# Performance work log

Measured on AMD Instinct MI355X. Metric: run time of the kernel, lower is better.

Reference implementation:

```python
import jax, jax.numpy as jnp
import numpy as np

B, T, I, H = 512, 64, 128, 128
E = I - 1  # encoder_in


def _cell(x, h, c, Wih, Whh, bih, bhh):
    # PyTorch LSTM gate order: i, f, g, o
    g = x @ Wih.T + h @ Whh.T + bih + bhh
    i, f, gg, o = jnp.split(g, 4, axis=-1)
    c2 = jax.nn.sigmoid(f) * c + jax.nn.sigmoid(i) * jnp.tanh(gg)
    h2 = jax.nn.sigmoid(o) * jnp.tanh(c2)
    return h2, c2


def setup_inputs() -> dict:
    key = jax.random.key(0)
    ks = iter(jax.random.split(key, 40))
    n = lambda *s: jax.random.normal(next(ks), s, dtype=jnp.float32) * 0.05
    inp = {
        'input_data': jax.random.normal(next(ks), (B, T, I), dtype=jnp.float32),
        # encoder LSTM (2 layers, input E)
        'enc_Wih0': n(4 * H, E), 'enc_Whh0': n(4 * H, H), 'enc_bih0': n(4 * H), 'enc_bhh0': n(4 * H),
        'enc_Wih1': n(4 * H, H), 'enc_Whh1': n(4 * H, H), 'enc_bih1': n(4 * H), 'enc_bhh1': n(4 * H),
        # decoder LSTM (2 layers, input 1)
        'dec_Wih0': n(4 * H, 1), 'dec_Whh0': n(4 * H, H), 'dec_bih0': n(4 * H), 'dec_bhh0': n(4 * H),
        'dec_Wih1': n(4 * H, H), 'dec_Whh1': n(4 * H, H), 'dec_bih1': n(4 * H), 'dec_bhh1': n(4 * H),
        # input attention MLP: (2H+T)->T->1
        'attn_W1': n(T, 2 * H + T), 'attn_b1': n(T), 'attn_W2': n(1, T), 'attn_b2': n(1),
        # temporal attention MLP: 3H->H->1
        'attnd_W1': n(H, 3 * H), 'attnd_b1': n(H), 'attnd_W2': n(1, H), 'attnd_b2': n(1),
        # decoder input projection (H+1)->1 and output projection 2H->1
        'decin_W': n(1, H + 1), 'decin_b': n(1),
        'proj_W': n(1, 2 * H), 'proj_b': n(1),
    }
    return inp


def reference(input_data, enc_Wih0, enc_Whh0, enc_bih0, enc_bhh0,
              enc_Wih1, enc_Whh1, enc_bih1, enc_bhh1,
              dec_Wih0, dec_Whh0, dec_bih0, dec_bhh0,
              dec_Wih1, dec_Whh1, dec_bih1, dec_bhh1,
              attn_W1, attn_b1, attn_W2, attn_b2,
              attnd_W1, attnd_b1, attnd_W2, attnd_b2,
              decin_W, decin_b, proj_W, proj_b):
    b, t, i = input_data.shape
    e, hdim = i - 1, enc_Whh0.shape[1]
    inp_enc = input_data[:, :, 1:]              # [B,T,E]
    inp_dec = input_data[:, :, 0]               # [B,T]
    inp_perm = jnp.transpose(inp_enc, (0, 2, 1))  # [B,E,T]
    z = jnp.zeros((b, hdim), input_data.dtype)

    def enc_step(carry, x_t):
        h0, c0, h1, c1 = carry
        hc = jnp.concatenate([
            jnp.broadcast_to(h1[:, None, :], (b, e, hdim)),
            jnp.broadcast_to(c1[:, None, :], (b, e, hdim)),
            inp_perm], axis=-1)                              # [B,E,2H+T]
        logits = jnp.tanh(hc @ attn_W1.T + attn_b1) @ attn_W2.T + attn_b2
        a = jax.nn.softmax(logits[..., 0], axis=-1)          # [B,E]
        h0, c0 = _cell(x_t * a, h0, c0, enc_Wih0, enc_Whh0, enc_bih0, enc_bhh0)
        h1, c1 = _cell(h0, h1, c1, enc_Wih1, enc_Whh1, enc_bih1, enc_bhh1)
        return (h0, c0, h1, c1), h1

    _, h_top = jax.lax.scan(enc_step, (z, z, z, z), jnp.transpose(inp_enc, (1, 0, 2)))
    h_exp = jnp.transpose(h_top, (1, 0, 2))  # [B,T,H]

    def dec_step(carry, x_t):
        h0, c0, h1, c1, _ = carry
        hc = jnp.concatenate([
            jnp.broadcast_to(h1[:, None, :], (b, t, hdim)),
            jnp.broadcast_to(c1[:, None, :], (b, t, hdim)),
            h_exp], axis=-1)                                  # [B,T,3H]
        logits = jnp.tanh(hc @ attnd_W1.T + attnd_b1) @ attnd_W2.T + attnd_b2
        a = jax.nn.softmax(logits[..., 0], axis=-1)           # [B,T]
        partial = jnp.einsum('bth,bt->bh', h_exp, a)          # [B,H]
        full = jnp.concatenate([partial, x_t[:, None]], axis=-1)  # [B,H+1]
        din = full @ decin_W.T + decin_b                      # [B,1]
        h0, c0 = _cell(din, h0, c0, dec_Wih0, dec_Whh0, dec_bih0, dec_bhh0)
        h1, c1 = _cell(h0, h1, c1, dec_Wih1, dec_Whh1, dec_bih1, dec_bhh1)
        return (h0, c0, h1, c1, partial), None

    (h0, c0, h1, c1, partial), _ = jax.lax.scan(dec_step, (z, z, z, z, z), jnp.transpose(inp_dec))
    out = jnp.concatenate([h1, partial], axis=-1) @ proj_W.T + proj_b  # [B,1]
    return out
```

## Files before the change

kernel.cpp:

```cpp
#include <hip/hip_runtime.h>

#define BATCH 512
#define TT 64
#define II 128

#define OFF_Wr_e0 0
#define OFF_Wr_e1 (OFF_Wr_e0 + 512*256)
#define OFF_Wr_d1 (OFF_Wr_e1 + 512*256)
#define OFF_bs0e  (OFF_Wr_d1 + 512*256)
#define OFF_bs1e  (OFF_bs0e + 512)
#define OFF_bs0d  (OFF_bs1e + 512)
#define OFF_bs1d  (OFF_bs0d + 512)
#define OFF_xprojT (OFF_bs1d + 512)
#define OFF_hexp   (OFF_xprojT + BATCH*8192)
#define OFF_hprojT (OFF_hexp + BATCH*8192)

struct Params {
  const float* input;
  const float *eWih0, *eWhh0, *ebih0, *ebhh0, *eWih1, *eWhh1, *ebih1, *ebhh1;
  const float *dWih0, *dWhh0, *dbih0, *dbhh0, *dWih1, *dWhh1, *dbih1, *dbhh1;
  const float *aW1, *ab1, *aW2, *ab2;
  const float *adW1, *adb1, *adW2, *adb2;
  const float *dinW, *dinb, *projW, *projb;
  float* ws;
  float* out;
};

#define L2E 1.4426950408889634f

__device__ __forceinline__ float exp2f_(float x){ return __builtin_amdgcn_exp2f(x); }
__device__ __forceinline__ float rcp_(float x){ return __builtin_amdgcn_rcpf(x); }
__device__ __forceinline__ float fast_tanh(float x){
  float t = exp2f_(x * 2.8853900817779268f);
  return 1.f - 2.f * rcp_(t + 1.f);
}
__device__ __forceinline__ float sigm(float x){
  return rcp_(1.f + exp2f_(-x * L2E));
}
__device__ __forceinline__ float wave_max(float v){
  #pragma unroll
  for (int o = 32; o > 0; o >>= 1) v = fmaxf(v, __shfl_xor(v, o, 64));
  return v;
}
__device__ __forceinline__ float wave_sum(float v){
  #pragma unroll
  for (int o = 32; o > 0; o >>= 1) v += __shfl_xor(v, o, 64);
  return v;
}

#define DOT(A,W,X) A += (W).x*(X).x + (W).y*(X).y + (W).z*(X).z + (W).w*(X).w;

__global__ __launch_bounds__(256) void k_prep(Params p){
  float* ws = p.ws;
  const int gid = blockIdx.x*256 + threadIdx.x;
  const int gsz = gridDim.x*256;
  for (int i = gid; i < 512*256; i += gsz){
    const int j = i >> 8, k = i & 255;
    ws[OFF_Wr_e0 + i] = (k < 128) ? ((k < 127) ? p.eWih0[j*127 + k] : 0.f)
                                  : p.eWhh0[j*128 + (k-128)];
    ws[OFF_Wr_e1 + i] = (k < 128) ? p.eWih1[j*128 + k] : p.eWhh1[j*128 + (k-128)];
    ws[OFF_Wr_d1 + i] = (k < 128) ? p.dWih1[j*128 + k] : p.dWhh1[j*128 + (k-128)];
  }
  for (int i = gid; i < 512; i += gsz){
    ws[OFF_bs0e+i] = p.ebih0[i]+p.ebhh0[i];
    ws[OFF_bs1e+i] = p.ebih1[i]+p.ebhh1[i];
    ws[OFF_bs0d+i] = p.dbih0[i]+p.dbhh0[i];
    ws[OFF_bs1d+i] = p.dbih1[i]+p.dbhh1[i];
  }
}

__global__ __launch_bounds__(256) void k_xproj(Params p){
  __shared__ float xin[64][128];
  __shared__ float w1x[64][64];
  __shared__ float b1s[64];
  const int b = blockIdx.x, tid = threadIdx.x;
  const float* inb = p.input + (size_t)b*(TT*II);
  for (int i = tid; i < 64*128; i += 256){
    const int k = i >> 7, e = i & 127;
    xin[k][e] = (e < 127) ? inb[k*II + 1 + e] : 0.f;
  }
  for (int i = tid; i < 64*64; i += 256){
    const int j = i >> 6, k = i & 63;
    w1x[j][k] = p.aW1[j*320 + 256 + k];
  }
  if (tid < 64) b1s[tid] = p.ab1[tid];
  __syncthreads();
  float* outb = p.ws + OFF_xprojT + (size_t)b*8192;
  for (int i = tid; i < 64*128; i += 256){
    const int j = i >> 7, e = i & 127;
    float acc = b1s[j];
    #pragma unroll 8
    for (int k = 0; k < 64; ++k) acc += xin[k][e] * w1x[j][k];
    outb[i] = acc;
  }
}

__global__ __launch_bounds__(256) void k_hproj(Params p){
  __shared__ float hx[64][129];
  __shared__ float bs[128];
  const int b = blockIdx.x, tid = threadIdx.x;
  const float* hb = p.ws + OFF_hexp + (size_t)b*8192;
  for (int i = tid; i < 64*128; i += 256) hx[i>>7][i&127] = hb[i];
  if (tid < 128) bs[tid] = p.adb1[tid];
  __syncthreads();
  float* outb = p.ws + OFF_hprojT + (size_t)b*8192;
  for (int i = tid; i < 128*64; i += 256){
    const int kk = i >> 6, t2 = i & 63;
    const float* w = p.adW1 + kk*384 + 256;
    float acc = bs[kk];
    #pragma unroll 8
    for (int k = 0; k < 128; ++k) acc += hx[t2][k] * w[k];
    outb[i] = acc;
  }
}

#define ENC_LDS_FLOATS (16384+1024+256+1024+1024+128+64+8+8)
__global__ __launch_bounds__(512) void k_enc(Params p){
  extern __shared__ float sm[];
  float* xp   = sm;
  float* Se   = xp + 16384;
  float* c0s  = Se + 1024;
  float* gpA  = c0s + 256;
  float* gpB  = gpA + 1024;
  float* g01s = gpB + 1024;
  float* w2   = g01s + 128;
  float* pm   = w2 + 64;
  float* psu  = pm + 8;
  const int tid = threadIdx.x;
  const int b0 = blockIdx.x*2;
  float* ws = p.ws;

  { const float4* xsrc = (const float4*)(ws + OFF_xprojT + (size_t)b0*8192);
    float4* xdst = (float4*)xp;
    for (int i = tid; i < 4096; i += 512) xdst[i] = xsrc[i]; }
  for (int i = tid; i < 1024; i += 512) Se[i] = 0.f;
  if (tid < 256) c0s[tid] = 0.f;
  if (tid < 64) w2[tid] = p.aW2[tid];
  const float b2 = p.ab2[0];

  const int kqE = tid & 3, oE = tid >> 2, jjE = oE & 63, bbE = oE >> 6;
  const int jh2 = tid & 1, o2 = tid >> 1, e2 = o2 & 127, bb2 = o2 >> 7;
  const int qtr = (tid >> 6) & 3;
  const int jg = tid & 255, khg = tid >> 8;
  const int uu = tid & 127, bbu = (tid >> 7) & 1;

  const float bias0a = ws[OFF_bs0e + jg], bias0b = ws[OFF_bs0e + 256 + jg];
  const float bias1a = ws[OFF_bs1e + jg], bias1b = ws[OFF_bs1e + 256 + jg];
  const float* wE1 = p.aW1 + jjE*320 + kqE*64;
  const float* wE3 = ws + OFF_Wr_e0 + jg*256 + khg*128;
  const float* wE4 = ws + OFF_Wr_e1 + jg*256 + khg*128;
  __syncthreads();

  for (int t = 0; t < TT; ++t){
    {
      const float* xbase = Se + bbE*512 + 256 + kqE*64;
      float a = 0.f;
      #pragma unroll
      for (int kg = 0; kg < 16; ++kg){
        const int idx = (((kg + kqE*4 + bbE*2) & 15) << 2);
        const float4 w = *(const float4*)(wE1 + idx);
        const float4 x = *(const float4*)(xbase + idx);
        DOT(a,w,x)
      }
      a += __shfl_xor(a,1,64); a += __shfl_xor(a,2,64);
      if (kqE == 0) g01s[bbE*64 + jjE] = a;
    }
    __syncthreads();
    float accL;
    {
      const float* xpe = xp + bb2*8192 + e2;
      const float* gg = g01s + bb2*64 + jh2*32;
      const float* w2p = w2 + jh2*32;
      float a = 0.f;
      #pragma unroll 8
      for (int q = 0; q < 32; ++q)
        a += w2p[q] * fast_tanh(xpe[(jh2*32+q)*128] + gg[q]);
      a += __shfl_xor(a,1,64);
      a += b2;
      if (e2 == 127) a = -3.0e38f;
      accL = a;
      const float m = wave_max(a);
      const float pe = exp2f_((a - m)*L2E);
      const float s = wave_sum(pe)*0.5f;
      if ((tid & 63) == 0){ pm[bb2*4+qtr] = m; psu[bb2*4+qtr] = s; }
    }
    __syncthreads();
    {
      const float m0=pm[bb2*4],m1=pm[bb2*4+1],m2=pm[bb2*4+2],m3=pm[bb2*4+3];
      const float gm = fmaxf(fmaxf(m0,m1),fmaxf(m2,m3));
      const float tot = psu[bb2*4]*exp2f_((m0-gm)*L2E) + psu[bb2*4+1]*exp2f_((m1-gm)*L2E)
                      + psu[bb2*4+2]*exp2f_((m2-gm)*L2E) + psu[bb2*4+3]*exp2f_((m3-gm)*L2E);
      const float aa = exp2f_((accL-gm)*L2E)*rcp_(tot);
      float xv = 0.f;
      if (e2 < 127) xv = p.input[(size_t)(b0+bb2)*8192 + t*128 + 1 + e2] * aa;
      Se[bb2*512 + e2] = xv;
    }
    __syncthreads();
    {
      const float* ob0 = Se + khg*128;
      const float* ob1 = Se + 512 + khg*128;
      float a00,a01,a10,a11;
      a00 = a01 = khg ? 0.f : bias0a;
      a10 = a11 = khg ? 0.f : bias0b;
      #pragma unroll 8
      for (int kg = 0; kg < 32; ++kg){
        const float4 w  = *(const float4*)(wE3 + kg*4);
        const float4 w2_= *(const float4*)(wE3 + 65536 + kg*4);
        const float4 x0 = *(const float4*)(ob0 + kg*4);
        const float4 x1 = *(const float4*)(ob1 + kg*4);
        DOT(a00,w,x0) DOT(a01,w,x1) DOT(a10,w2_,x0) DOT(a11,w2_,x1)
      }
      float* gp = khg ? gpB : gpA;
      gp[jg] = a00; gp[512 + jg] = a01;
      gp[256 + jg] = a10; gp[768 + jg] = a11;
    }
    __syncthreads();
    if (tid < 256){
      const int base = bbu*512 + uu;
      const float gi = gpA[base] + gpB[base];
      const float gf = gpA[base+128] + gpB[base+128];
      const float gg2= gpA[base+256] + gpB[base+256];
      const float go = gpA[base+384] + gpB[base+384];
      const float c = sigm(gf)*c0s[tid] + sigm(gi)*fast_tanh(gg2);
      c0s[tid] = c;
      Se[bbu*512 + 128 + uu] = sigm(go)*fast_tanh(c);
    }
    __syncthreads();
    {
      const float* ob0 = Se + 128 + khg*128;
      const float* ob1 = Se + 640 + khg*128;
      float a00,a01,a10,a11;
      a00 = a01 = khg ? 0.f : bias1a;
      a10 = a11 = khg ? 0.f : bias1b;
      #pragma unroll 8
      for (int kg = 0; kg < 32; ++kg){
        const float4 w  = *(const float4*)(wE4 + kg*4);
        const float4 w2_= *(const float4*)(wE4 + 65536 + kg*4);
        const float4 x0 = *(const float4*)(ob0 + kg*4);
        const float4 x1 = *(const float4*)(ob1 + kg*4);
        DOT(a00,w,x0) DOT(a01,w,x1) DOT(a10,w2_,x0) DOT(a11,w2_,x1)
      }
      float* gp = khg ? gpB : gpA;
      gp[jg] = a00; gp[512 + jg] = a01;
      gp[256 + jg] = a10; gp[768 + jg] = a11;
    }
    __syncthreads();
    if (tid < 256){
      const int base = bbu*512 + uu;
      const float gi = gpA[base] + gpB[base];
      const float gf = gpA[base+128] + gpB[base+128];
      const float gg2= gpA[base+256] + gpB[base+256];
      const float go = gpA[base+384] + gpB[base+384];
      const float c = sigm(gf)*Se[bbu*512+384+uu] + sigm(gi)*fast_tanh(gg2);
      Se[bbu*512+384+uu] = c;
      const float h = sigm(go)*fast_tanh(c);
      Se[bbu*512+256+uu] = h;
      ws[OFF_hexp + (size_t)(b0+bbu)*8192 + t*128 + uu] = h;
    }
    __syncthreads();
  }
}

#define DEC_LDS_FLOATS (16640+768+256+1024+1024+256+128+8+8+8+128+256)
__global__ __launch_bounds__(512) void k_dec(Params p){
  extern __shared__ float sm[];
  float* hp    = sm;
  float* Sd    = hp + 16640;
  float* c0s   = Sd + 768;
  float* gpA   = c0s + 256;
  float* gpB   = gpA + 1024;
  float* g01d  = gpB + 1024;
  float* lraw  = g01d + 256;
  float* pm    = lraw + 128;
  float* psu   = pm + 8;
  float* dpart = psu + 8;
  float* wd2   = dpart + 8;
  float* parts = wd2 + 128;
  const int tid = threadIdx.x;
  const int b0 = blockIdx.x*2;
  float* ws = p.ws;

  { const float* hsrc = ws + OFF_hprojT + (size_t)b0*8192;
    for (int i = tid; i < 16384; i += 512){
      const int bb = i>>13, kk = (i>>6)&127, tl = i&63;
      hp[bb*8320 + kk*65 + tl] = hsrc[i];
    } }
  for (int i = tid; i < 768; i += 512) Sd[i] = 0.f;
  if (tid < 256) c0s[tid] = 0.f;
  if (tid < 128) wd2[tid] = p.adW2[tid];
  const float bd2 = p.adb2[0];

  const int kh1 = tid & 1, o1 = tid >> 1, kk1 = o1 & 127, bb1 = o1 >> 7;
  const int kqa = tid & 3, oa = tid >> 2, tla = oa & 63, bba = oa >> 6;
  const int qtr = (tid >> 6) & 3;
  const int thc = tid & 1, oc = tid >> 1, hc = oc & 127, bbc = oc >> 7;
  const int jg = tid & 255, khg = tid >> 8;
  const int uu = tid & 127, bbu = (tid >> 7) & 1;

  const float bias0da = ws[OFF_bs0d + jg], bias0db = ws[OFF_bs0d + 256 + jg];
  const float bias1da = ws[OFF_bs1d + jg], bias1db = ws[OFF_bs1d + 256 + jg];
  const float dW0a = p.dWih0[jg], dW0b = p.dWih0[256 + jg];
  const float dinw_hc = p.dinW[hc];
  const float dinw128 = p.dinW[128], dinbv = p.dinb[0];
  const float* wD1 = p.adW1 + kk1*384 + kh1*128;
  const float* wD3 = p.dWhh0 + jg*128 + khg*64;
  const float* wD4 = ws + OFF_Wr_d1 + jg*256 + khg*128;
  const float* heB = ws + OFF_hexp + (size_t)(b0+bbc)*8192 + hc;
  __syncthreads();

  for (int t = 0; t < TT; ++t){
    {
      const float* xbase = Sd + bb1*384 + 128 + kh1*128;
      float a = 0.f;
      #pragma unroll 8
      for (int kg = 0; kg < 32; ++kg){
        const int idx = (((kg + kh1*4 + bb1*2) & 31) << 2);
        const float4 w = *(const float4*)(wD1 + idx);
        const float4 x = *(const float4*)(xbase + idx);
        DOT(a,w,x)
      }
      a += __shfl_xor(a,1,64);
      if (kh1 == 0) g01d[bb1*128 + kk1] = a;
    }
    __syncthreads();
    {
      const float* hpb = hp + bba*8320 + tla;
      const float* gg = g01d + bba*128;
      float a = 0.f;
      #pragma unroll 8
      for (int q = 0; q < 32; ++q){
        const int kk = kqa*32 + ((q + kqa*8) & 31);
        a += wd2[kk] * fast_tanh(hpb[kk*65] + gg[kk]);
      }
      a += __shfl_xor(a,1,64); a += __shfl_xor(a,2,64);
      a += bd2;
      if (kqa == 0) lraw[bba*64 + tla] = a;
      const float m = wave_max(a);
      const float pe = exp2f_((a-m)*L2E);
      const float s = wave_sum(pe)*0.25f;
      if ((tid & 63) == 0){ pm[bba*4+qtr] = m; psu[bba*4+qtr] = s; }
    }
    __syncthreads();
    if (tid < 128){
      const int bb = tid >> 6;
      const float m0=pm[bb*4],m1=pm[bb*4+1],m2=pm[bb*4+2],m3=pm[bb*4+3];
      const float gm = fmaxf(fmaxf(m0,m1),fmaxf(m2,m3));
      const float tot = psu[bb*4]*exp2f_((m0-gm)*L2E)+psu[bb*4+1]*exp2f_((m1-gm)*L2E)
                      +psu[bb*4+2]*exp2f_((m2-gm)*L2E)+psu[bb*4+3]*exp2f_((m3-gm)*L2E);
      lraw[tid] = exp2f_((lraw[tid]-gm)*L2E)*rcp_(tot);
    }
    __syncthreads();
    {
      const float* av = lraw + bbc*64 + thc*32;
      float a = 0.f;
      #pragma unroll 8
      for (int q = 0; q < 32; ++q) a += av[q] * heB[(thc*32+q)*128];
      a += __shfl_xor(a,1,64);
      if (thc == 0) parts[bbc*128 + hc] = a;
      float v = a * dinw_hc;
      v = wave_sum(v)*0.5f;
      if ((tid & 63) == 0) dpart[bbc*4+qtr] = v;
    }
    __syncthreads();
    {
      const float dn0 = dpart[0]+dpart[1]+dpart[2]+dpart[3]
                      + p.input[(size_t)(b0+0)*8192 + t*128]*dinw128 + dinbv;
      const float dn1 = dpart[4]+dpart[5]+dpart[6]+dpart[7]
                      + p.input[(size_t)(b0+1)*8192 + t*128]*dinw128 + dinbv;
      const float* ob0 = Sd + khg*64;
      const float* ob1 = Sd + 384 + khg*64;
      float a00,a01,a10,a11;
      if (khg){ a00=a01=a10=a11=0.f; }
      else {
        a00 = bias0da + dn0*dW0a; a01 = bias0da + dn1*dW0a;
        a10 = bias0db + dn0*dW0b; a11 = bias0db + dn1*dW0b;
      }
      #pragma unroll 8
      for (int kg = 0; kg < 16; ++kg){
        const float4 w  = *(const float4*)(wD3 + kg*4);
        const float4 w2_= *(const float4*)(wD3 + 32768 + kg*4);
        const float4 x0 = *(const float4*)(ob0 + kg*4);
        const float4 x1 = *(const float4*)(ob1 + kg*4);
        DOT(a00,w,x0) DOT(a01,w,x1) DOT(a10,w2_,x0) DOT(a11,w2_,x1)
      }
      float* gp = khg ? gpB : gpA;
      gp[jg] = a00; gp[512 + jg] = a01;
      gp[256 + jg] = a10; gp[768 + jg] = a11;
    }
    __syncthreads();
    if (tid < 256){
      const int base = bbu*512 + uu;
      const float gi = gpA[base] + gpB[base];
      const float gf = gpA[base+128] + gpB[base+128];
      const float gg2= gpA[base+256] + gpB[base+256];
      const float go = gpA[base+384] + gpB[base+384];
      const float c = sigm(gf)*c0s[tid] + sigm(gi)*fast_tanh(gg2);
      c0s[tid] = c;
      Sd[bbu*384 + uu] = sigm(go)*fast_tanh(c);
    }
    __syncthreads();
    {
      const float* ob0 = Sd + khg*128;
      const float* ob1 = Sd + 384 + khg*128;
      float a00,a01,a10,a11;
      a00 = a01 = khg ? 0.f : bias1da;
      a10 = a11 = khg ? 0.f : bias1db;
      #pragma unroll 8
      for (int kg = 0; kg < 32; ++kg){
        const float4 w  = *(const float4*)(wD4 + kg*4);
        const float4 w2_= *(const float4*)(wD4 + 65536 + kg*4);
        const float4 x0 = *(const float4*)(ob0 + kg*4);
        const float4 x1 = *(const float4*)(ob1 + kg*4);
        DOT(a00,w,x0) DOT(a01,w,x1) DOT(a10,w2_,x0) DOT(a11,w2_,x1)
      }
      float* gp = khg ? gpB : gpA;
      gp[jg] = a00; gp[512 + jg] = a01;
      gp[256 + jg] = a10; gp[768 + jg] = a11;
    }
    __syncthreads();
    if (tid < 256){
      const int base = bbu*512 + uu;
      const float gi = gpA[base] + gpB[base];
      const float gf = gpA[base+128] + gpB[base+128];
      const float gg2= gpA[base+256] + gpB[base+256];
      const float go = gpA[base+384] + gpB[base+384];
      const float c = sigm(gf)*Sd[bbu*384+256+uu] + sigm(gi)*fast_tanh(gg2);
      Sd[bbu*384+256+uu] = c;
      Sd[bbu*384+128+uu] = sigm(go)*fast_tanh(c);
    }
    __syncthreads();
  }
  if (tid < 128){
    const int bb = tid>>6, l = tid&63;
    float v = Sd[bb*384+128+l]*p.projW[l] + Sd[bb*384+192+l]*p.projW[64+l]
            + parts[bb*128+l]*p.projW[128+l] + parts[bb*128+64+l]*p.projW[192+l];
    v = wave_sum(v);
    if (l == 0) p.out[b0 + bb] = v + p.projb[0];
  }
}

extern "C" void kernel_launch(void* const* d_in, const int* in_sizes, int n_in,
                              void* d_out, int out_size, void* d_ws, size_t ws_size,
                              hipStream_t stream){
  Params p;
  p.input = (const float*)d_in[0];
  p.eWih0=(const float*)d_in[1];  p.eWhh0=(const float*)d_in[2];
  p.ebih0=(const float*)d_in[3];  p.ebhh0=(const float*)d_in[4];
  p.eWih1=(const float*)d_in[5];  p.eWhh1=(const float*)d_in[6];
  p.ebih1=(const float*)d_in[7];  p.ebhh1=(const float*)d_in[8];
  p.dWih0=(const float*)d_in[9];  p.dWhh0=(const float*)d_in[10];
  p.dbih0=(const float*)d_in[11]; p.dbhh0=(const float*)d_in[12];
  p.dWih1=(const float*)d_in[13]; p.dWhh1=(const float*)d_in[14];
  p.dbih1=(const float*)d_in[15]; p.dbhh1=(const float*)d_in[16];
  p.aW1=(const float*)d_in[17];   p.ab1=(const float*)d_in[18];
  p.aW2=(const float*)d_in[19];   p.ab2=(const float*)d_in[20];
  p.adW1=(const float*)d_in[21];  p.adb1=(const float*)d_in[22];
  p.adW2=(const float*)d_in[23];  p.adb2=(const float*)d_in[24];
  p.dinW=(const float*)d_in[25];  p.dinb=(const float*)d_in[26];
  p.projW=(const float*)d_in[27]; p.projb=(const float*)d_in[28];
  p.ws = (float*)d_ws;
  p.out = (float*)d_out;

  (void)hipFuncSetAttribute(reinterpret_cast<const void*>(k_enc),
      hipFuncAttributeMaxDynamicSharedMemorySize, ENC_LDS_FLOATS*4);
  (void)hipFuncSetAttribute(reinterpret_cast<const void*>(k_dec),
      hipFuncAttributeMaxDynamicSharedMemorySize, DEC_LDS_FLOATS*4);

  hipLaunchKernelGGL(k_prep,  dim3(128), dim3(256), 0, stream, p);
  hipLaunchKernelGGL(k_xproj, dim3(BATCH), dim3(256), 0, stream, p);
  hipLaunchKernelGGL(k_enc,   dim3(256), dim3(512), ENC_LDS_FLOATS*4, stream, p);
  hipLaunchKernelGGL(k_hproj, dim3(BATCH), dim3(256), 0, stream, p);
  hipLaunchKernelGGL(k_dec,   dim3(256), dim3(512), DEC_LDS_FLOATS*4, stream, p);
}
```

Before: 4.872 ms.

## Hold recurrent LSTM weights in registers with one batch per 1024-thread block

The encoder and decoder recurrent kernels now handle one batch element per block with 1024 threads instead of two per 512-thread block. Each thread preloads its slice of the LSTM and attention weights into registers once, so the inner loops no longer re-read weights from global memory at every timestep. The decoder also stages h_exp in LDS instead of reading it from global memory. The cost is very high register pressure (about 68 float4 per thread), which risks spills and leaves little occupancy. Reductions are spread over more threads, with extra scratch passes through LDS.

```diff
diff --git a/kernel.cpp b/kernel.cpp
--- a/kernel.cpp
+++ b/kernel.cpp
@@ -114,328 +114,276 @@
   }
 }
 
-#define ENC_LDS_FLOATS (16384+1024+256+1024+1024+128+64+8+8)
-__global__ __launch_bounds__(512) void k_enc(Params p){
+#define ENC_LDS_FLOATS (8192+512+128+512+512+1024+64+64+2+2)
+__global__ __launch_bounds__(1024) void k_enc(Params p){
   extern __shared__ float sm[];
   float* xp   = sm;
-  float* Se   = xp + 16384;
-  float* c0s  = Se + 1024;
-  float* gpA  = c0s + 256;
-  float* gpB  = gpA + 1024;
-  float* g01s = gpB + 1024;
-  float* w2   = g01s + 128;
-  float* pm   = w2 + 64;
-  float* psu  = pm + 8;
+  float* Se   = xp + 8192;
+  float* c0s  = Se + 512;
+  float* gpA  = c0s + 128;
+  float* gpB  = gpA + 512;
+  float* scr  = gpB + 512;
+  float* g01  = scr + 1024;
+  float* w2s  = g01 + 64;
+  float* pm   = w2s + 64;
+  float* psu  = pm + 2;
   const int tid = threadIdx.x;
-  const int b0 = blockIdx.x*2;
+  const int b = blockIdx.x;
   float* ws = p.ws;
 
-  { const float4* xsrc = (const float4*)(ws + OFF_xprojT + (size_t)b0*8192);
-    float4* xdst = (float4*)xp;
-    for (int i = tid; i < 4096; i += 512) xdst[i] = xsrc[i]; }
-  for (int i = tid; i < 1024; i += 512) Se[i] = 0.f;
-  if (tid < 256) c0s[tid] = 0.f;
-  if (tid < 64) w2[tid] = p.aW2[tid];
+  { const float4* s = (const float4*)(ws + OFF_xprojT + (size_t)b*8192);
+    float4* d = (float4*)xp;
+    d[tid] = s[tid];
+    d[tid + 1024] = s[tid + 1024]; }
+  if (tid < 512) Se[tid] = 0.f;
+  if (tid < 128) c0s[tid] = 0.f;
+  if (tid < 64) w2s[tid] = p.aW2[tid];
   const float b2 = p.ab2[0];
 
-  const int kqE = tid & 3, oE = tid >> 2, jjE = oE & 63, bbE = oE >> 6;
-  const int jh2 = tid & 1, o2 = tid >> 1, e2 = o2 & 127, bb2 = o2 >> 7;
-  const int qtr = (tid >> 6) & 3;
-  const int jg = tid & 255, khg = tid >> 8;
-  const int uu = tid & 127, bbu = (tid >> 7) & 1;
-
-  const float bias0a = ws[OFF_bs0e + jg], bias0b = ws[OFF_bs0e + 256 + jg];
-  const float bias1a = ws[OFF_bs1e + jg], bias1b = ws[OFF_bs1e + 256 + jg];
-  const float* wE1 = p.aW1 + jjE*320 + kqE*64;
-  const float* wE3 = ws + OFF_Wr_e0 + jg*256 + khg*128;
-  const float* wE4 = ws + OFF_Wr_e1 + jg*256 + khg*128;
+  const int kqE = tid & 15, jjE = tid >> 4;
+  const int eA = tid & 127, jq = tid >> 7;
+  const int r = tid & 511, kh = tid >> 9;
+
+  float4 W1[4], W3[32], W4[32];
+  #pragma unroll
+  for (int i = 0; i < 4; ++i)
+    W1[i] = *(const float4*)(p.aW1 + jjE*320 + kqE*16 + ((i + kqE) & 3)*4);
+  #pragma unroll
+  for (int i = 0; i < 32; ++i)
+    W3[i] = *(const float4*)(ws + OFF_Wr_e0 + r*256 + kh*128 + i*4);
+  #pragma unroll
+  for (int i = 0; i < 32; ++i)
+    W4[i] = *(const float4*)(ws + OFF_Wr_e1 + r*256 + kh*128 + i*4);
+  const float bias0 = ws[OFF_bs0e + r];
+  const float bias1 = ws[OFF_bs1e + r];
+  const float* xrow = p.input + (size_t)b*8192;
   __syncthreads();
 
   for (int t = 0; t < TT; ++t){
-    {
-      const float* xbase = Se + bbE*512 + 256 + kqE*64;
-      float a = 0.f;
-      #pragma unroll
-      for (int kg = 0; kg < 16; ++kg){
-        const int idx = (((kg + kqE*4 + bbE*2) & 15) << 2);
-        const float4 w = *(const float4*)(wE1 + idx);
-        const float4 x = *(const float4*)(xbase + idx);
-        DOT(a,w,x)
+    float xreg = 0.f;
+    if (tid < 127) xreg = xrow[t*128 + 1 + tid];
+    {
+      const float4* X = (const float4*)(Se + 256) + kqE*4;
+      float a = 0.f;
+      #pragma unroll
+      for (int i = 0; i < 4; ++i){ const float4 x = X[(i + kqE) & 3]; DOT(a, W1[i], x) }
+      a += __shfl_xor(a,1,64); a += __shfl_xor(a,2,64);
+      a += __shfl_xor(a,4,64); a += __shfl_xor(a,8,64);
+      if (kqE == 0) g01[jjE] = a;
+    }
+    __syncthreads();
+    {
+      float a = 0.f;
+      #pragma unroll
+      for (int q = 0; q < 8; ++q){
+        const int j = jq*8 + q;
+        a += w2s[j] * fast_tanh(xp[j*128 + eA] + g01[j]);
       }
-      a += __shfl_xor(a,1,64); a += __shfl_xor(a,2,64);
-      if (kqE == 0) g01s[bbE*64 + jjE] = a;
-    }
-    __syncthreads();
-    float accL;
-    {
-      const float* xpe = xp + bb2*8192 + e2;
-      const float* gg = g01s + bb2*64 + jh2*32;
-      const float* w2p = w2 + jh2*32;
-      float a = 0.f;
-      #pragma unroll 8
-      for (int q = 0; q < 32; ++q)
-        a += w2p[q] * fast_tanh(xpe[(jh2*32+q)*128] + gg[q]);
-      a += __shfl_xor(a,1,64);
-      a += b2;
-      if (e2 == 127) a = -3.0e38f;
-      accL = a;
+      scr[jq*128 + eA] = a;
+    }
+    __syncthreads();
+    float aL = 0.f;
+    if (tid < 128){
+      aL = b2;
+      #pragma unroll
+      for (int q = 0; q < 8; ++q) aL += scr[q*128 + tid];
+      if (tid == 127) aL = -3.0e38f;
+      const float m = wave_max(aL);
+      const float pe = exp2f_((aL - m)*L2E);
+      const float s = wave_sum(pe);
+      if ((tid & 63) == 0){ pm[tid>>6] = m; psu[tid>>6] = s; }
+    }
+    __syncthreads();
+    if (tid < 128){
+      const float m0 = pm[0], m1 = pm[1];
+      const float gm = fmaxf(m0, m1);
+      const float tot = psu[0]*exp2f_((m0-gm)*L2E) + psu[1]*exp2f_((m1-gm)*L2E);
+      const float aa = exp2f_((aL-gm)*L2E)*rcp_(tot);
+      Se[tid] = (tid < 127) ? xreg*aa : 0.f;
+    }
+    __syncthreads();
+    {
+      float a = kh ? 0.f : bias0;
+      const float4* X = (const float4*)Se + kh*32;
+      #pragma unroll
+      for (int kg = 0; kg < 32; ++kg){ const float4 x = X[kg]; DOT(a, W3[kg], x) }
+      (kh ? gpB : gpA)[r] = a;
+    }
+    __syncthreads();
+    if (tid < 128){
+      const float gi = gpA[tid]+gpB[tid], gf = gpA[128+tid]+gpB[128+tid];
+      const float gg = gpA[256+tid]+gpB[256+tid], go = gpA[384+tid]+gpB[384+tid];
+      const float c = sigm(gf)*c0s[tid] + sigm(gi)*fast_tanh(gg);
+      c0s[tid] = c;
+      Se[128+tid] = sigm(go)*fast_tanh(c);
+    }
+    __syncthreads();
+    {
+      float a = kh ? 0.f : bias1;
+      const float4* X = (const float4*)Se + 32 + kh*32;
+      #pragma unroll
+      for (int kg = 0; kg < 32; ++kg){ const float4 x = X[kg]; DOT(a, W4[kg], x) }
+      (kh ? gpB : gpA)[r] = a;
+    }
+    __syncthreads();
+    if (tid < 128){
+      const float gi = gpA[tid]+gpB[tid], gf = gpA[128+tid]+gpB[128+tid];
+      const float gg = gpA[256+tid]+gpB[256+tid], go = gpA[384+tid]+gpB[384+tid];
+      const float c = sigm(gf)*Se[384+tid] + sigm(gi)*fast_tanh(gg);
+      Se[384+tid] = c;
+      const float h = sigm(go)*fast_tanh(c);
+      Se[256+tid] = h;
+      ws[OFF_hexp + (size_t)b*8192 + t*128 + tid] = h;
+    }
+    __syncthreads();
+  }
+}
+
+#define DEC_LDS_FLOATS (8320+8192+384+128+512+512+1024+128+64+128+2+128)
+__global__ __launch_bounds__(1024) void k_dec(Params p){
+  extern __shared__ float sm[];
+  float* hp    = sm;
+  float* hex   = hp + 8320;
+  float* Sd    = hex + 8192;
+  float* c0s   = Sd + 384;
+  float* gpA   = c0s + 128;
+  float* gpB   = gpA + 512;
+  float* scr   = gpB + 512;
+  float* g01d  = scr + 1024;
+  float* abuf  = g01d + 128;
+  float* parts = abuf + 64;
+  float* dpart = parts + 128;
+  float* wd2   = dpart + 2;
+  const int tid = threadIdx.x;
+  const int b = blockIdx.x;
+  float* ws = p.ws;
+
+  { const float* s = ws + OFF_hprojT + (size_t)b*8192;
+    #pragma unroll
+    for (int rep = 0; rep < 8; ++rep){
+      const int i = rep*1024 + tid;
+      hp[(i>>6)*65 + (i&63)] = s[i];
+    }
+    const float4* s2 = (const float4*)(ws + OFF_hexp + (size_t)b*8192);
+    ((float4*)hex)[tid] = s2[tid];
+    ((float4*)hex)[tid + 1024] = s2[tid + 1024];
+  }
+  if (tid < 384) Sd[tid] = 0.f;
+  if (tid < 128) c0s[tid] = 0.f;
+  if (tid < 128) wd2[tid] = p.adW2[tid];
+  const float bd2 = p.adb2[0];
+
+  const int kq8 = tid & 7, kkD = tid >> 3;
+  const int tA = tid & 63, kq16 = tid >> 6;
+  const int hC = tid & 127, tq = tid >> 7;
+  const int r = tid & 511, kh = tid >> 9;
+
+  float4 WD1[8], WD3[16], WD4[32];
+  #pragma unroll
+  for (int i = 0; i < 8; ++i)
+    WD1[i] = *(const float4*)(p.adW1 + kkD*384 + kq8*32 + ((i + kq8) & 7)*4);
+  #pragma unroll
+  for (int i = 0; i < 16; ++i)
+    WD3[i] = *(const float4*)(p.dWhh0 + r*128 + kh*64 + i*4);
+  #pragma unroll
+  for (int i = 0; i < 32; ++i)
+    WD4[i] = *(const float4*)(ws + OFF_Wr_d1 + r*256 + kh*128 + i*4);
+  const float bias0d = ws[OFF_bs0d + r];
+  const float bias1d = ws[OFF_bs1d + r];
+  const float dW0r = p.dWih0[r];
+  const float dinw_h = p.dinW[hC];
+  const float dinw128 = p.dinW[128], dinbv = p.dinb[0];
+  __syncthreads();
+
+  for (int t = 0; t < TT; ++t){
+    const float xd = p.input[(size_t)b*8192 + t*128];
+    {
+      const float4* X = (const float4*)(Sd + 128) + kq8*8;
+      float a = 0.f;
+      #pragma unroll
+      for (int i = 0; i < 8; ++i){ const float4 x = X[(i + kq8) & 7]; DOT(a, WD1[i], x) }
+      a += __shfl_xor(a,1,64); a += __shfl_xor(a,2,64); a += __shfl_xor(a,4,64);
+      if (kq8 == 0) g01d[kkD] = a;
+    }
+    __syncthreads();
+    {
+      float a = 0.f;
+      #pragma unroll
+      for (int q = 0; q < 8; ++q){
+        const int kk = kq16*8 + q;
+        a += wd2[kk] * fast_tanh(hp[kk*65 + tA] + g01d[kk]);
+      }
+      scr[kq16*64 + tA] = a;
+    }
+    __syncthreads();
+    if (tid < 64){
+      float a = bd2;
+      #pragma unroll
+      for (int q = 0; q < 16; ++q) a += scr[q*64 + tid];
       const float m = wave_max(a);
       const float pe = exp2f_((a - m)*L2E);
-      const float s = wave_sum(pe)*0.5f;
-      if ((tid & 63) == 0){ pm[bb2*4+qtr] = m; psu[bb2*4+qtr] = s; }
-    }
-    __syncthreads();
-    {
-      const float m0=pm[bb2*4],m1=pm[bb2*4+1],m2=pm[bb2*4+2],m3=pm[bb2*4+3];
-      const float gm = fmaxf(fmaxf(m0,m1),fmaxf(m2,m3));
-      const float tot = psu[bb2*4]*exp2f_((m0-gm)*L2E) + psu[bb2*4+1]*exp2f_((m1-gm)*L2E)
-                      + psu[bb2*4+2]*exp2f_((m2-gm)*L2E) + psu[bb2*4+3]*exp2f_((m3-gm)*L2E);
-      const float aa = exp2f_((accL-gm)*L2E)*rcp_(tot);
-      float xv = 0.f;
-      if (e2 < 127) xv = p.input[(size_t)(b0+bb2)*8192 + t*128 + 1 + e2] * aa;
-      Se[bb2*512 + e2] = xv;
-    }
-    __syncthreads();
-    {
-      const float* ob0 = Se + khg*128;
-      const float* ob1 = Se + 512 + khg*128;
-      float a00,a01,a10,a11;
-      a00 = a01 = khg ? 0.f : bias0a;
-      a10 = a11 = khg ? 0.f : bias0b;
-      #pragma unroll 8
-      for (int kg = 0; kg < 32; ++kg){
-        const float4 w  = *(const float4*)(wE3 + kg*4);
-        const float4 w2_= *(const float4*)(wE3 + 65536 + kg*4);
-        const float4 x0 = *(const float4*)(ob0 + kg*4);
-        const float4 x1 = *(const float4*)(ob1 + kg*4);
-        DOT(a00,w,x0) DOT(a01,w,x1) DOT(a10,w2_,x0) DOT(a11,w2_,x1)
+      abuf[tid] = pe * rcp_(wave_sum(pe));
+    }
+    __syncthreads();
+    {
+      float a = 0.f;
+      #pragma unroll
+      for (int q = 0; q < 8; ++q){
+        const int t2 = tq*8 + q;
+        a += abuf[t2] * hex[t2*128 + hC];
       }
-      float* gp = khg ? gpB : gpA;
-      gp[jg] = a00; gp[512 + jg] = a01;
-      gp[256 + jg] = a10; gp[768 + jg] = a11;
-    }
-    __syncthreads();
-    if (tid < 256){
-      const int base = bbu*512 + uu;
-      const float gi = gpA[base] + gpB[base];
-      const float gf = gpA[base+128] + gpB[base+128];
-      const float gg2= gpA[base+256] + gpB[base+256];
-      const float go = gpA[base+384] + gpB[base+384];
-      const float c = sigm(gf)*c0s[tid] + sigm(gi)*fast_tanh(gg2);
+      scr[tq*128 + hC] = a;
+    }
+    __syncthreads();
+    if (tid < 128){
+      float a = 0.f;
+      #pragma unroll
+      for (int q = 0; q < 8; ++q) a += scr[q*128 + tid];
+      parts[tid] = a;
+      float v = a * dinw_h;
+      v = wave_sum(v);
+      if ((tid & 63) == 0) dpart[tid>>6] = v;
+    }
+    __syncthreads();
+    {
+      const float dn = dpart[0] + dpart[1] + xd*dinw128 + dinbv;
+      float a = kh ? 0.f : (bias0d + dn*dW0r);
+      const float4* X = (const float4*)Sd + kh*16;
+      #pragma unroll
+      for (int kg = 0; kg < 16; ++kg){ const float4 x = X[kg]; DOT(a, WD3[kg], x) }
+      (kh ? gpB : gpA)[r] = a;
+    }
+    __syncthreads();
+    if (tid < 128){
+      const float gi = gpA[tid]+gpB[tid], gf = gpA[128+tid]+gpB[128+tid];
+      const float gg = gpA[256+tid]+gpB[256+tid], go = gpA[384+tid]+gpB[384+tid];
+      const float c = sigm(gf)*c0s[tid] + sigm(gi)*fast_tanh(gg);
       c0s[tid] = c;
-      Se[bbu*512 + 128 + uu] = sigm(go)*fast_tanh(c);
-    }
-    __syncthreads();
-    {
-      const float* ob0 = Se + 128 + khg*128;
-      const float* ob1 = Se + 640 + khg*128;
-      float a00,a01,a10,a11;
-      a00 = a01 = khg ? 0.f : bias1a;
-      a10 = a11 = khg ? 0.f : bias1b;
-      #pragma unroll 8
-      for (int kg = 0; kg < 32; ++kg){
-        const float4 w  = *(const float4*)(wE4 + kg*4);
-        const float4 w2_= *(const float4*)(wE4 + 65536 + kg*4);
-        const float4 x0 = *(const float4*)(ob0 + kg*4);
-        const float4 x1 = *(const float4*)(ob1 + kg*4);
-        DOT(a00,w,x0) DOT(a01,w,x1) DOT(a10,w2_,x0) DOT(a11,w2_,x1)
-      }
-      float* gp = khg ? gpB : gpA;
-      gp[jg] = a00; gp[512 + jg] = a01;
-      gp[256 + jg] = a10; gp[768 + jg] = a11;
-    }
-    __syncthreads();
-    if (tid < 256){
-      const int base = bbu*512 + uu;
-      const float gi = gpA[base] + gpB[base];
-      const float gf = gpA[base+128] + gpB[base+128];
-      const float gg2= gpA[base+256] + gpB[base+256];
-      const float go = gpA[base+384] + gpB[base+384];
-      const float c = sigm(gf)*Se[bbu*512+384+uu] + sigm(gi)*fast_tanh(gg2);
-      Se[bbu*512+384+uu] = c;
-      const float h = sigm(go)*fast_tanh(c);
-      Se[bbu*512+256+uu] = h;
-      ws[OFF_hexp + (size_t)(b0+bbu)*8192 + t*128 + uu] = h;
-    }
-    __syncthreads();
-  }
-}
-
-#define DEC_LDS_FLOATS (16640+768+256+1024+1024+256+128+8+8+8+128+256)
-__global__ __launch_bounds__(512) void k_dec(Params p){
-  extern __shared__ float sm[];
-  float* hp    = sm;
-  float* Sd    = hp + 16640;
-  float* c0s   = Sd + 768;
-  float* gpA   = c0s + 256;
-  float* gpB   = gpA + 1024;
-  float* g01d  = gpB + 1024;
-  float* lraw  = g01d + 256;
-  float* pm    = lraw + 128;
-  float* psu   = pm + 8;
-  float* dpart = psu + 8;
-  float* wd2   = dpart + 8;
-  float* parts = wd2 + 128;
-  const int tid = threadIdx.x;
-  const int b0 = blockIdx.x*2;
-  float* ws = p.ws;
-
-  { const float* hsrc = ws + OFF_hprojT + (size_t)b0*8192;
-    for (int i = tid; i < 16384; i += 512){
-      const int bb = i>>13, kk = (i>>6)&127, tl = i&63;
-      hp[bb*8320 + kk*65 + tl] = hsrc[i];
-    } }
-  for (int i = tid; i < 768; i += 512) Sd[i] = 0.f;
-  if (tid < 256) c0s[tid] = 0.f;
-  if (tid < 128) wd2[tid] = p.adW2[tid];
-  const float bd2 = p.adb2[0];
-
-  const int kh1 = tid & 1, o1 = tid >> 1, kk1 = o1 & 127, bb1 = o1 >> 7;
-  const int kqa = tid & 3, oa = tid >> 2, tla = oa & 63, bba = oa >> 6;
-  const int qtr = (tid >> 6) & 3;
-  const int thc = tid & 1, oc = tid >> 1, hc = oc & 127, bbc = oc >> 7;
-  const int jg = tid & 255, khg = tid >> 8;
-  const int uu = tid & 127, bbu = (tid >> 7) & 1;
-
-  const float bias0da = ws[OFF_bs0d + jg], bias0db = ws[OFF_bs0d + 256 + jg];
-  const float bias1da = ws[OFF_bs1d + jg], bias1db = ws[OFF_bs1d + 256 + jg];
-  const float dW0a = p.dWih0[jg], dW0b = p.dWih0[256 + jg];
-  const float dinw_hc = p.dinW[hc];
-  const float dinw128 = p.dinW[128], dinbv = p.dinb[0];
-  const float* wD1 = p.adW1 + kk1*384 + kh1*128;
-  const float* wD3 = p.dWhh0 + jg*128 + khg*64;
-  const float* wD4 = ws + OFF_Wr_d1 + jg*256 + khg*128;
-  const float* heB = ws + OFF_hexp + (size_t)(b0+bbc)*8192 + hc;
-  __syncthreads();
-
-  for (int t = 0; t < TT; ++t){
-    {
-      const float* xbase = Sd + bb1*384 + 128 + kh1*128;
-      float a = 0.f;
-      #pragma unroll 8
-      for (int kg = 0; kg < 32; ++kg){
-        const int idx = (((kg + kh1*4 + bb1*2) & 31) << 2);
-        const float4 w = *(const float4*)(wD1 + idx);
-        const float4 x = *(const float4*)(xbase + idx);
-        DOT(a,w,x)
-      }
-      a += __shfl_xor(a,1,64);
-      if (kh1 == 0) g01d[bb1*128 + kk1] = a;
-    }
-    __syncthreads();
-    {
-      const float* hpb = hp + bba*8320 + tla;
-      const float* gg = g01d + bba*128;
-      float a = 0.f;
-      #pragma unroll 8
-      for (int q = 0; q < 32; ++q){
-        const int kk = kqa*32 + ((q + kqa*8) & 31);
-        a += wd2[kk] * fast_tanh(hpb[kk*65] + gg[kk]);
-      }
-      a += __shfl_xor(a,1,64); a += __shfl_xor(a,2,64);
-      a += bd2;
-      if (kqa == 0) lraw[bba*64 + tla] = a;
-      const float m = wave_max(a);
-      const float pe = exp2f_((a-m)*L2E);
-      const float s = wave_sum(pe)*0.25f;
-      if ((tid & 63) == 0){ pm[bba*4+qtr] = m; psu[bba*4+qtr] = s; }
-    }
-    __syncthreads();
-    if (tid < 128){
-      const int bb = tid >> 6;
-      const float m0=pm[bb*4],m1=pm[bb*4+1],m2=pm[bb*4+2],m3=pm[bb*4+3];
-      const float gm = fmaxf(fmaxf(m0,m1),fmaxf(m2,m3));
-      const float tot = psu[bb*4]*exp2f_((m0-gm)*L2E)+psu[bb*4+1]*exp2f_((m1-gm)*L2E)
-                      +psu[bb*4+2]*exp2f_((m2-gm)*L2E)+psu[bb*4+3]*exp2f_((m3-gm)*L2E);
-      lraw[tid] = exp2f_((lraw[tid]-gm)*L2E)*rcp_(tot);
-    }
-    __syncthreads();
-    {
-      const float* av = lraw + bbc*64 + thc*32;
-      float a = 0.f;
-      #pragma unroll 8
-      for (int q = 0; q < 32; ++q) a += av[q] * heB[(thc*32+q)*128];
-      a += __shfl_xor(a,1,64);
-      if (thc == 0) parts[bbc*128 + hc] = a;
-      float v = a * dinw_hc;
-      v = wave_sum(v)*0.5f;
-      if ((tid & 63) == 0) dpart[bbc*4+qtr] = v;
-    }
-    __syncthreads();
-    {
-      const float dn0 = dpart[0]+dpart[1]+dpart[2]+dpart[3]
-                      + p.input[(size_t)(b0+0)*8192 + t*128]*dinw128 + dinbv;
-      const float dn1 = dpart[4]+dpart[5]+dpart[6]+dpart[7]
-                      + p.input[(size_t)(b0+1)*8192 + t*128]*dinw128 + dinbv;
-      const float* ob0 = Sd + khg*64;
-      const float* ob1 = Sd + 384 + khg*64;
-      float a00,a01,a10,a11;
-      if (khg){ a00=a01=a10=a11=0.f; }
-      else {
-        a00 = bias0da + dn0*dW0a; a01 = bias0da + dn1*dW0a;
-        a10 = bias0db + dn0*dW0b; a11 = bias0db + dn1*dW0b;
-      }
-      #pragma unroll 8
-      for (int kg = 0; kg < 16; ++kg){
-        const float4 w  = *(const float4*)(wD3 + kg*4);
-        const float4 w2_= *(const float4*)(wD3 + 32768 + kg*4);
-        const float4 x0 = *(const float4*)(ob0 + kg*4);
-        const float4 x1 = *(const float4*)(ob1 + kg*4);
-        DOT(a00,w,x0) DOT(a01,w,x1) DOT(a10,w2_,x0) DOT(a11,w2_,x1)
-      }
-      float* gp = khg ? gpB : gpA;
-      gp[jg] = a00; gp[512 + jg] = a01;
-      gp[256 + jg] = a10; gp[768 + jg] = a11;
-    }
-    __syncthreads();
-    if (tid < 256){
-      const int base = bbu*512 + uu;
-      const float gi = gpA[base] + gpB[base];
-      const float gf = gpA[base+128] + gpB[base+128];
-      const float gg2= gpA[base+256] + gpB[base+256];
-      const float go = gpA[base+384] + gpB[base+384];
-      const float c = sigm(gf)*c0s[tid] + sigm(gi)*fast_tanh(gg2);
-      c0s[tid] = c;
-      Sd[bbu*384 + uu] = sigm(go)*fast_tanh(c);
-    }
-    __syncthreads();
-    {
-      const float* ob0 = Sd + khg*128;
-      const float* ob1 = Sd + 384 + khg*128;
-      float a00,a01,a10,a11;
-      a00 = a01 = khg ? 0.f : bias1da;
-      a10 = a11 = khg ? 0.f : bias1db;
-      #pragma unroll 8
-      for (int kg = 0; kg < 32; ++kg){
-        const float4 w  = *(const float4*)(wD4 + kg*4);
-        const float4 w2_= *(const float4*)(wD4 + 65536 + kg*4);
-        const float4 x0 = *(const float4*)(ob0 + kg*4);
-        const float4 x1 = *(const float4*)(ob1 + kg*4);
-        DOT(a00,w,x0) DOT(a01,w,x1) DOT(a10,w2_,x0) DOT(a11,w2_,x1)
-      }
-      float* gp = khg ? gpB : gpA;
-      gp[jg] = a00; gp[512 + jg] = a01;
-      gp[256 + jg] = a10; gp[768 + jg] = a11;
-    }
-    __syncthreads();
-    if (tid < 256){
-      const int base = bbu*512 + uu;
-      const float gi = gpA[base] + gpB[base];
-      const float gf = gpA[base+128] + gpB[base+128];
-      const float gg2= gpA[base+256] + gpB[base+256];
-      const float go = gpA[base+384] + gpB[base+384];
-      const float c = sigm(gf)*Sd[bbu*384+256+uu] + sigm(gi)*fast_tanh(gg2);
-      Sd[bbu*384+256+uu] = c;
-      Sd[bbu*384+128+uu] = sigm(go)*fast_tanh(c);
-    }
-    __syncthreads();
-  }
-  if (tid < 128){
-    const int bb = tid>>6, l = tid&63;
-    float v = Sd[bb*384+128+l]*p.projW[l] + Sd[bb*384+192+l]*p.projW[64+l]
-            + parts[bb*128+l]*p.projW[128+l] + parts[bb*128+64+l]*p.projW[192+l];
+      Sd[tid] = sigm(go)*fast_tanh(c);
+    }
+    __syncthreads();
+    {
+      float a = kh ? 0.f : bias1d;
+      const float4* X = (const float4*)Sd + kh*32;
+      #pragma unroll
+      for (int kg = 0; kg < 32; ++kg){ const float4 x = X[kg]; DOT(a, WD4[kg], x) }
+      (kh ? gpB : gpA)[r] = a;
+    }
+    __syncthreads();
+    if (tid < 128){
+      const float gi = gpA[tid]+gpB[tid], gf = gpA[128+tid]+gpB[128+tid];
+      const float gg = gpA[256+tid]+gpB[256+tid], go = gpA[384+tid]+gpB[384+tid];
+      const float c = sigm(gf)*Sd[256+tid] + sigm(gi)*fast_tanh(gg);
+      Sd[256+tid] = c;
+      Sd[128+tid] = sigm(go)*fast_tanh(c);
+    }
+    __syncthreads();
+  }
+  if (tid < 64){
+    float v = Sd[128+tid]*p.projW[tid] + Sd[192+tid]*p.projW[64+tid]
+            + parts[tid]*p.projW[128+tid] + parts[64+tid]*p.projW[192+tid];
     v = wave_sum(v);
-    if (l == 0) p.out[b0 + bb] = v + p.projb[0];
+    if (tid == 0) p.out[b] = v + p.projb[0];
   }
 }
 
@@ -468,7 +416,7 @@
 
   hipLaunchKernelGGL(k_prep,  dim3(128), dim3(256), 0, stream, p);
   hipLaunchKernelGGL(k_xproj, dim3(BATCH), dim3(256), 0, stream, p);
-  hipLaunchKernelGGL(k_enc,   dim3(256), dim3(512), ENC_LDS_FLOATS*4, stream, p);
+  hipLaunchKernelGGL(k_enc,   dim3(BATCH), dim3(1024), ENC_LDS_FLOATS*4, stream, p);
   hipLaunchKernelGGL(k_hproj, dim3(BATCH), dim3(256), 0, stream, p);
-  hipLaunchKernelGGL(k_dec,   dim3(256), dim3(512), DEC_LDS_FLOATS*4, stream, p);
-}
+  hipLaunchKernelGGL(k_dec,   dim3(BATCH), dim3(1024), DEC_LDS_FLOATS*4, stream, p);
+}
```

Measured after the change: 8.798 ms. +80.6%, slower.
